# Kernel optimization log

Measured on AMD Instinct MI355X. Metric: run time of the kernel, lower is better.

The kernel has to match this reference:

```python
import jax, jax.numpy as jnp
import numpy as np

B, S, D, DK, DV = 8, 2048, 256, 128, 128

def setup_inputs() -> dict:
    key = jax.random.key(0)
    ks = jax.random.split(key, 9)
    return {
        "x_q": jax.random.normal(ks[0], (B, S, D), jnp.float32),
        "x_k": jax.random.normal(ks[1], (B, S, D), jnp.float32),
        "x_v": jax.random.normal(ks[2], (B, S, D), jnp.float32),
        "Wq": jax.random.normal(ks[3], (D, DK), jnp.float32) * (1.0 / np.sqrt(D)),
        "bq": jax.random.normal(ks[4], (DK,), jnp.float32) * 0.02,
        "Wk": jax.random.normal(ks[5], (D, DK), jnp.float32) * (1.0 / np.sqrt(D)),
        "bk": jax.random.normal(ks[6], (DK,), jnp.float32) * 0.02,
        "Wv": jax.random.normal(ks[7], (D, DV), jnp.float32) * (1.0 / np.sqrt(D)),
        "bv": jax.random.normal(ks[8], (DV,), jnp.float32) * 0.02,
    }

def reference(x_q, x_k, x_v, Wq, bq, Wk, bk, Wv, bv):
    # Dense projections: [B,S,D] @ [D,dk] + bias
    q = jnp.einsum("bsd,dk->bsk", x_q, Wq) + bq
    k = jnp.einsum("bsd,dk->bsk", x_k, Wk) + bk
    v = jnp.einsum("bsd,dv->bsv", x_v, Wv) + bv
    scale = 1.0 / np.sqrt(Wq.shape[1]).astype(np.float32)  # 1/sqrt(d_k)
    scores = jnp.einsum("bqk,bsk->bqs", q, k) * scale       # [B,S,S]
    attn = jax.nn.softmax(scores, axis=-1)
    return jnp.einsum("bqs,bsv->bqv", attn, v)               # [B,S,d_v]
```

## Files before the change

kernel.cpp:

```cpp
#include <hip/hip_runtime.h>
#include <stdint.h>

typedef float    f32x4 __attribute__((ext_vector_type(4)));
typedef _Float16 f16x8 __attribute__((ext_vector_type(8)));
typedef _Float16 f16x4 __attribute__((ext_vector_type(4)));
typedef unsigned int u32x4 __attribute__((ext_vector_type(4)));

#define SPLIT 4
#define NTILES 8

__device__ __forceinline__ f32x4 mfma16(f16x8 a, f16x8 b, f32x4 c) {
    return __builtin_amdgcn_mfma_f32_16x16x32_f16(a, b, c, 0, 0, 0);
}
__device__ __forceinline__ f32x4 mfma16k16(f16x4 a, f16x4 b, f32x4 c) {
    return __builtin_amdgcn_mfma_f32_16x16x16f16(a, b, c, 0, 0, 0);
}

__global__ __launch_bounds__(256) void prep_weights(
    const float* __restrict__ Wq, const float* __restrict__ Wk,
    const float* __restrict__ Wv, _Float16* __restrict__ wt) {
    __shared__ float Ls[64 * 65];
    const int bx = blockIdx.x;
    const int w  = bx >> 3, t = bx & 7;
    const int k0 = (t >> 1) * 64, n0 = (t & 1) * 64;
    const float* W = (w == 0) ? Wq : (w == 1) ? Wk : Wv;
    const int tid = threadIdx.x;
    #pragma unroll
    for (int i = 0; i < 16; i++) {
        int idx = i * 256 + tid;
        int r = idx >> 6, c = idx & 63;
        Ls[r * 65 + c] = W[(k0 + r) * 128 + n0 + c];
    }
    __syncthreads();
    #pragma unroll
    for (int i = 0; i < 16; i++) {
        int idx = i * 256 + tid;
        int r2 = idx >> 6, c2 = idx & 63;
        wt[w * 32768 + (n0 + r2) * 256 + k0 + c2] = (_Float16)Ls[c2 * 65 + r2];
    }
}

__global__ __launch_bounds__(256) void proj_kernel(
    const float* __restrict__ xq, const float* __restrict__ xk,
    const float* __restrict__ xv, const _Float16* __restrict__ wt,
    const float* __restrict__ bq, const float* __restrict__ bk,
    const float* __restrict__ bv,
    _Float16* __restrict__ qo, _Float16* __restrict__ ko,
    _Float16* __restrict__ vtmp)
{
    const int mode = blockIdx.y;
    const float*    X    = mode == 0 ? xq : mode == 1 ? xk : xv;
    const float*    bias = mode == 0 ? bq : mode == 1 ? bk : bv;
    const _Float16* W    = wt + mode * 32768;
    _Float16*       Y    = mode == 0 ? qo : mode == 1 ? ko : vtmp;

    const int tid  = threadIdx.x;
    const int wave = tid >> 6, lane = tid & 63;
    const int ln   = lane & 15, qd = lane >> 4;
    const int row0 = blockIdx.x * 64 + wave * 16;

    const float*    xrow = X + (size_t)(row0 + ln) * 256 + qd * 8;
    const _Float16* wb   = W + ln * 256 + qd * 8;

    f32x4 acc[8];
    #pragma unroll
    for (int i = 0; i < 8; i++) acc[i] = (f32x4){0.f, 0.f, 0.f, 0.f};

    #pragma unroll
    for (int kk = 0; kk < 8; kk++) {
        f32x4 a0 = *(const f32x4*)(xrow + kk * 32);
        f32x4 a1 = *(const f32x4*)(xrow + kk * 32 + 4);
        f16x8 af;
        af[0] = (_Float16)a0[0]; af[1] = (_Float16)a0[1];
        af[2] = (_Float16)a0[2]; af[3] = (_Float16)a0[3];
        af[4] = (_Float16)a1[0]; af[5] = (_Float16)a1[1];
        af[6] = (_Float16)a1[2]; af[7] = (_Float16)a1[3];
        #pragma unroll
        for (int nt = 0; nt < 8; nt++) {
            f16x8 bf = *(const f16x8*)(wb + nt * 4096 + kk * 32);
            acc[nt] = mfma16(af, bf, acc[nt]);
        }
    }

    const float SC = 0.08838834764831845f * 1.4426950408889634f;
    #pragma unroll
    for (int nt = 0; nt < 8; nt++) {
        int col = nt * 16 + ln;
        float bb = bias[col];
        #pragma unroll
        for (int r = 0; r < 4; r++) {
            int orow = row0 + qd * 4 + r;
            float val = acc[nt][r] + bb;
            if (mode == 0) val *= SC;
            Y[(size_t)orow * 128 + col] = (_Float16)val;
        }
    }
}

__global__ __launch_bounds__(256) void transpose_v(
    const _Float16* __restrict__ vtmp, _Float16* __restrict__ vt)
{
    __shared__ __align__(16) _Float16 Ls[64 * 72];
    const int b  = blockIdx.z;
    const int s0 = blockIdx.x * 64;
    const int d0 = blockIdx.y * 64;
    const int tid = threadIdx.x;
    #pragma unroll
    for (int i = 0; i < 2; i++) {
        int idx = i * 256 + tid;
        int r = idx >> 3, c = (idx & 7) * 8;
        *(f16x8*)&Ls[r * 72 + c] =
            *(const f16x8*)(vtmp + (size_t)(b * 2048 + s0 + r) * 128 + d0 + c);
    }
    __syncthreads();
    #pragma unroll
    for (int i = 0; i < 2; i++) {
        int idx = i * 256 + tid;
        int dr = idx >> 3, sc8 = (idx & 7) * 8;
        f16x8 o;
        #pragma unroll
        for (int j = 0; j < 8; j++) o[j] = Ls[(sc8 + j) * 72 + dr];
        *(f16x8*)(vt + (size_t)(b * 128 + d0 + dr) * 2048 + s0 + sc8) = o;
    }
}

__global__ __launch_bounds__(512, 4) void attn_kernel(
    const _Float16* __restrict__ qp, const _Float16* __restrict__ kp,
    const _Float16* __restrict__ vtp, _Float16* __restrict__ opart,
    float2* __restrict__ ml)
{
    const int bid = blockIdx.x;
    const int gx  = bid & 7;
    const int q0i = (bid >> 3) & 15;
    const int gg  = bid >> 7;
    const int g   = gg * 8 + gx;
    const int b   = g >> 2;
    const int z   = g & 3;
    const int q0  = q0i * 128;

    const int tid  = threadIdx.x;
    const int wave = tid >> 6, lane = tid & 63;
    const int ln   = lane & 15, qd = lane >> 4;

    __shared__ __align__(16) _Float16 smem[17920];
    _Float16* Ks = smem;
    _Float16* Vs = smem + 8704;

    const _Float16* qrow =
        qp + (size_t)(b * 2048 + q0 + wave * 16 + ln) * 128 + qd * 8;
    f16x8 qf[4];
    #pragma unroll
    for (int c = 0; c < 4; c++) qf[c] = *(const f16x8*)(qrow + c * 32);

    f32x4 o[8];
    #pragma unroll
    for (int i = 0; i < 8; i++) o[i] = (f32x4){0.f, 0.f, 0.f, 0.f};
    float m_run = -1e30f, l_run = 0.f;

    const _Float16* kbase = kp + (size_t)b * 2048 * 128;
    const _Float16* vbase = vtp + (size_t)b * 128 * 2048;

    for (int kt = z * NTILES; kt < z * NTILES + NTILES; kt++) {
        __syncthreads();
        const _Float16* ks = kbase + kt * 64 * 128;
        #pragma unroll
        for (int i = tid; i < 1024; i += 512) {
            int r = i >> 4, c = i & 15;
            *(u32x4*)&Ks[r * 136 + c * 8] = *(const u32x4*)(ks + r * 128 + c * 8);
        }
        const _Float16* vs = vbase + kt * 64;
        #pragma unroll
        for (int i = tid; i < 1024; i += 512) {
            int r = i >> 3, c = i & 7;
            *(u32x4*)&Vs[r * 72 + c * 8] =
                *(const u32x4*)(vs + (size_t)r * 2048 + c * 8);
        }
        __syncthreads();

        f32x4 sc[4];
        #pragma unroll
        for (int st = 0; st < 4; st++) {
            sc[st] = (f32x4){0.f, 0.f, 0.f, 0.f};
            int base = (st * 16 + ln) * 136 + qd * 8;
            #pragma unroll
            for (int c = 0; c < 4; c++) {
                f16x8 kf = *(const f16x8*)&Ks[base + c * 32];
                sc[st] = mfma16(kf, qf[c], sc[st]);
            }
        }

        float t = sc[0][0];
        #pragma unroll
        for (int st = 0; st < 4; st++)
            #pragma unroll
            for (int r = 0; r < 4; r++) t = fmaxf(t, sc[st][r]);
        t = fmaxf(t, __shfl_xor(t, 16));
        t = fmaxf(t, __shfl_xor(t, 32));
        const float mnew  = fmaxf(m_run, t);
        const float alpha = exp2f(m_run - mnew);

        f16x4 ph[4];
        float ssum = 0.f;
        #pragma unroll
        for (int st = 0; st < 4; st++) {
            #pragma unroll
            for (int r = 0; r < 4; r++) {
                float p = exp2f(sc[st][r] - mnew);
                ssum += p;
                ph[st][r] = (_Float16)p;
            }
        }
        ssum += __shfl_xor(ssum, 16);
        ssum += __shfl_xor(ssum, 32);
        l_run = l_run * alpha + ssum;
        m_run = mnew;

        #pragma unroll
        for (int dt = 0; dt < 8; dt++)
            #pragma unroll
            for (int r = 0; r < 4; r++) o[dt][r] *= alpha;

        #pragma unroll
        for (int st = 0; st < 4; st++) {
            #pragma unroll
            for (int dt = 0; dt < 8; dt++) {
                f16x4 vf = *(const f16x4*)&Vs[(dt * 16 + ln) * 72 + st * 16 + qd * 4];
                o[dt] = mfma16k16(vf, ph[st], o[dt]);
            }
        }
    }

    __syncthreads();
    _Float16* pw = smem + wave * 2176;
    #pragma unroll
    for (int dt = 0; dt < 8; dt++) {
        f16x4 h;
        #pragma unroll
        for (int r = 0; r < 4; r++) h[r] = (_Float16)o[dt][r];
        *(f16x4*)&pw[ln * 136 + dt * 16 + qd * 4] = h;
    }
    const size_t prow = (size_t)(z * 8 + b) * 2048 + q0 + wave * 16;
    __builtin_amdgcn_s_waitcnt(0);
    #pragma unroll
    for (int i = 0; i < 4; i++) {
        int row = i * 4 + qd;
        f16x8 vrow = *(const f16x8*)&pw[row * 136 + ln * 8];
        *(f16x8*)(opart + (prow + row) * 128 + ln * 8) = vrow;
    }
    if (qd == 0) {
        float2 v; v.x = m_run; v.y = l_run;
        ml[prow + ln] = v;
    }
}

__global__ __launch_bounds__(256) void merge_kernel(
    const _Float16* __restrict__ opart, const float2* __restrict__ ml,
    float* __restrict__ out)
{
    const int t = threadIdx.x;
    const int r = t >> 4, cg = t & 15;
    const size_t row = (size_t)blockIdx.x * 16 + r;

    float M = -1e30f;
    #pragma unroll
    for (int zi = 0; zi < SPLIT; zi++)
        M = fmaxf(M, ml[(size_t)zi * 16384 + row].x);
    float L = 0.f;
    float acc[8] = {0.f, 0.f, 0.f, 0.f, 0.f, 0.f, 0.f, 0.f};
    #pragma unroll
    for (int zi = 0; zi < SPLIT; zi++) {
        float2 p = ml[(size_t)zi * 16384 + row];
        float w = exp2f(p.x - M);
        L += w * p.y;
        f16x8 v = *(const f16x8*)&opart[((size_t)zi * 16384 + row) * 128 + cg * 8];
        #pragma unroll
        for (int j = 0; j < 8; j++) acc[j] += w * (float)v[j];
    }
    const float inv = 1.0f / L;
    float* op = out + row * 128 + cg * 8;
    f32x4 lo = (f32x4){acc[0] * inv, acc[1] * inv, acc[2] * inv, acc[3] * inv};
    f32x4 hi = (f32x4){acc[4] * inv, acc[5] * inv, acc[6] * inv, acc[7] * inv};
    *(f32x4*)op = lo;
    *(f32x4*)(op + 4) = hi;
}

extern "C" void kernel_launch(void* const* d_in, const int* in_sizes, int n_in,
                              void* d_out, int out_size, void* d_ws, size_t ws_size,
                              hipStream_t stream) {
    const float* xq = (const float*)d_in[0];
    const float* xk = (const float*)d_in[1];
    const float* xv = (const float*)d_in[2];
    const float* Wq = (const float*)d_in[3];
    const float* bq = (const float*)d_in[4];
    const float* Wk = (const float*)d_in[5];
    const float* bk = (const float*)d_in[6];
    const float* Wv = (const float*)d_in[7];
    const float* bv = (const float*)d_in[8];
    float* out = (float*)d_out;

    char* ws = (char*)d_ws;
    _Float16* wt    = (_Float16*)ws;
    _Float16* qo    = (_Float16*)(ws + 196608);
    _Float16* ko    = (_Float16*)(ws + 196608 + 4194304);
    _Float16* vt    = (_Float16*)(ws + 196608 + 2 * 4194304);
    float2*   ml    = (float2*)  (ws + 196608 + 3 * 4194304);
    _Float16* opart = (_Float16*)(ws + 196608 + 3 * 4194304 + 1048576);
    _Float16* vtmp  = opart;

    hipLaunchKernelGGL(prep_weights, dim3(24), dim3(256), 0, stream,
                       Wq, Wk, Wv, wt);
    hipLaunchKernelGGL(proj_kernel, dim3(256, 3), dim3(256), 0, stream,
                       xq, xk, xv, wt, bq, bk, bv, qo, ko, vtmp);
    hipLaunchKernelGGL(transpose_v, dim3(32, 2, 8), dim3(256), 0, stream,
                       vtmp, vt);
    hipLaunchKernelGGL(attn_kernel, dim3(16 * 8 * SPLIT), dim3(512), 0, stream,
                       qo, ko, vt, opart, ml);
    hipLaunchKernelGGL(merge_kernel, dim3(1024), dim3(256), 0, stream,
                       opart, ml, out);
}
```

Before: 166.9 us.

## Halve attention block size and register-prefetch next K/V tile

The attention kernel now uses 256-thread blocks covering 64 query rows, so the grid doubles to 1024 blocks. The next K and V tile is loaded from global memory into registers while the current tile is computed, hiding global load latency behind the MFMA work. The output rescale by alpha is skipped when the running max did not change anywhere in the wave. In exchange, each K/V tile is loaded from global memory by twice as many blocks, and the prefetch buffers raise register pressure.

```diff
diff --git a/kernel.cpp b/kernel.cpp
--- a/kernel.cpp
+++ b/kernel.cpp
@@ -124,19 +124,19 @@
     }
 }
 
-__global__ __launch_bounds__(512, 4) void attn_kernel(
+__global__ __launch_bounds__(256, 4) void attn_kernel(
     const _Float16* __restrict__ qp, const _Float16* __restrict__ kp,
     const _Float16* __restrict__ vtp, _Float16* __restrict__ opart,
     float2* __restrict__ ml)
 {
     const int bid = blockIdx.x;
     const int gx  = bid & 7;
-    const int q0i = (bid >> 3) & 15;
-    const int gg  = bid >> 7;
+    const int q0i = (bid >> 3) & 31;
+    const int gg  = bid >> 8;
     const int g   = gg * 8 + gx;
     const int b   = g >> 2;
     const int z   = g & 3;
-    const int q0  = q0i * 128;
+    const int q0  = q0i * 64;
 
     const int tid  = threadIdx.x;
     const int wave = tid >> 6, lane = tid & 63;
@@ -160,22 +160,38 @@
     const _Float16* kbase = kp + (size_t)b * 2048 * 128;
     const _Float16* vbase = vtp + (size_t)b * 128 * 2048;
 
-    for (int kt = z * NTILES; kt < z * NTILES + NTILES; kt++) {
+    const int kt0 = z * NTILES;
+    u32x4 kpre[4], vpre[4];
+    {
+        const _Float16* ks = kbase + (size_t)kt0 * 64 * 128;
+        const _Float16* vs = vbase + kt0 * 64;
+        #pragma unroll
+        for (int j = 0; j < 4; j++) {
+            int i = j * 256 + tid;
+            kpre[j] = *(const u32x4*)(ks + (i >> 4) * 128 + (i & 15) * 8);
+            vpre[j] = *(const u32x4*)(vs + (size_t)(i >> 3) * 2048 + (i & 7) * 8);
+        }
+    }
+
+    for (int kt = kt0; kt < kt0 + NTILES; kt++) {
         __syncthreads();
-        const _Float16* ks = kbase + kt * 64 * 128;
-        #pragma unroll
-        for (int i = tid; i < 1024; i += 512) {
-            int r = i >> 4, c = i & 15;
-            *(u32x4*)&Ks[r * 136 + c * 8] = *(const u32x4*)(ks + r * 128 + c * 8);
-        }
-        const _Float16* vs = vbase + kt * 64;
-        #pragma unroll
-        for (int i = tid; i < 1024; i += 512) {
-            int r = i >> 3, c = i & 7;
-            *(u32x4*)&Vs[r * 72 + c * 8] =
-                *(const u32x4*)(vs + (size_t)r * 2048 + c * 8);
+        #pragma unroll
+        for (int j = 0; j < 4; j++) {
+            int i = j * 256 + tid;
+            *(u32x4*)&Ks[(i >> 4) * 136 + (i & 15) * 8] = kpre[j];
+            *(u32x4*)&Vs[(i >> 3) * 72 + (i & 7) * 8]   = vpre[j];
         }
         __syncthreads();
+        if (kt + 1 < kt0 + NTILES) {
+            const _Float16* ks = kbase + (size_t)(kt + 1) * 64 * 128;
+            const _Float16* vs = vbase + (kt + 1) * 64;
+            #pragma unroll
+            for (int j = 0; j < 4; j++) {
+                int i = j * 256 + tid;
+                kpre[j] = *(const u32x4*)(ks + (i >> 4) * 128 + (i & 15) * 8);
+                vpre[j] = *(const u32x4*)(vs + (size_t)(i >> 3) * 2048 + (i & 7) * 8);
+            }
+        }
 
         f32x4 sc[4];
         #pragma unroll
@@ -215,10 +231,12 @@
         l_run = l_run * alpha + ssum;
         m_run = mnew;
 
-        #pragma unroll
-        for (int dt = 0; dt < 8; dt++)
-            #pragma unroll
-            for (int r = 0; r < 4; r++) o[dt][r] *= alpha;
+        if (__any(alpha != 1.0f)) {
+            #pragma unroll
+            for (int dt = 0; dt < 8; dt++)
+                #pragma unroll
+                for (int r = 0; r < 4; r++) o[dt][r] *= alpha;
+        }
 
         #pragma unroll
         for (int st = 0; st < 4; st++) {
@@ -313,7 +331,7 @@
                        xq, xk, xv, wt, bq, bk, bv, qo, ko, vtmp);
     hipLaunchKernelGGL(transpose_v, dim3(32, 2, 8), dim3(256), 0, stream,
                        vtmp, vt);
-    hipLaunchKernelGGL(attn_kernel, dim3(16 * 8 * SPLIT), dim3(512), 0, stream,
+    hipLaunchKernelGGL(attn_kernel, dim3(32 * 8 * SPLIT), dim3(256), 0, stream,
                        qo, ko, vt, opart, ml);
     hipLaunchKernelGGL(merge_kernel, dim3(1024), dim3(256), 0, stream,
                        opart, ml, out);
```

Measured after the change: 210.4 us. +26.1%, slower.

## Double-buffer K/V tiles via async global-to-LDS loads with XOR swizzle

Applied to the files above, without the earlier changes.

Replaces the synchronous register-staged K/V tile copies with `global_load_lds` direct-to-LDS loads into two buffers. The next tile is prefetched while the current one is computed, which also removes one barrier per iteration. LDS padding is replaced by XOR-swizzled addressing on both the store and read sides to avoid bank conflicts. Shared memory grows from about 35KB to 64KB per block, which can cut the number of resident blocks per CU and so reduce latency hiding.

```diff
diff --git a/kernel.cpp b/kernel.cpp
--- a/kernel.cpp
+++ b/kernel.cpp
@@ -14,6 +14,11 @@
 }
 __device__ __forceinline__ f32x4 mfma16k16(f16x4 a, f16x4 b, f32x4 c) {
     return __builtin_amdgcn_mfma_f32_16x16x16f16(a, b, c, 0, 0, 0);
+}
+__device__ __forceinline__ void gll16(const _Float16* g, _Float16* l) {
+    __builtin_amdgcn_global_load_lds(
+        (const __attribute__((address_space(1))) void*)g,
+        (__attribute__((address_space(3))) void*)l, 16, 0, 0);
 }
 
 __global__ __launch_bounds__(256) void prep_weights(
@@ -142,9 +147,7 @@
     const int wave = tid >> 6, lane = tid & 63;
     const int ln   = lane & 15, qd = lane >> 4;
 
-    __shared__ __align__(16) _Float16 smem[17920];
-    _Float16* Ks = smem;
-    _Float16* Vs = smem + 8704;
+    __shared__ __align__(16) _Float16 smem[32768];
 
     const _Float16* qrow =
         qp + (size_t)(b * 2048 + q0 + wave * 16 + ln) * 128 + qd * 8;
@@ -159,32 +162,41 @@
 
     const _Float16* kbase = kp + (size_t)b * 2048 * 128;
     const _Float16* vbase = vtp + (size_t)b * 128 * 2048;
-
-    for (int kt = z * NTILES; kt < z * NTILES + NTILES; kt++) {
+    const int kt0 = z * NTILES;
+
+    auto stage = [&](int kt, int buf) {
+        const _Float16* ks = kbase + (size_t)kt * 64 * 128;
+        const _Float16* vs = vbase + kt * 64;
+        _Float16* kdst0 = smem + buf * 8192;
+        _Float16* vdst0 = smem + 16384 + buf * 8192;
+        #pragma unroll
+        for (int j = 0; j < 2; j++) {
+            int p  = wave * 128 + j * 64 + lane;
+            int r  = p >> 4, cp = p & 15;
+            int cl = cp ^ (r & 15);
+            gll16(ks + r * 128 + cl * 8, kdst0 + (wave * 128 + j * 64) * 8);
+            int dv = p >> 3, cq = p & 7;
+            int c2 = cq ^ (dv & 7);
+            gll16(vs + (size_t)dv * 2048 + c2 * 8, vdst0 + (wave * 128 + j * 64) * 8);
+        }
+    };
+
+    stage(kt0, 0);
+
+    for (int it = 0; it < NTILES; it++) {
         __syncthreads();
-        const _Float16* ks = kbase + kt * 64 * 128;
-        #pragma unroll
-        for (int i = tid; i < 1024; i += 512) {
-            int r = i >> 4, c = i & 15;
-            *(u32x4*)&Ks[r * 136 + c * 8] = *(const u32x4*)(ks + r * 128 + c * 8);
-        }
-        const _Float16* vs = vbase + kt * 64;
-        #pragma unroll
-        for (int i = tid; i < 1024; i += 512) {
-            int r = i >> 3, c = i & 7;
-            *(u32x4*)&Vs[r * 72 + c * 8] =
-                *(const u32x4*)(vs + (size_t)r * 2048 + c * 8);
-        }
-        __syncthreads();
+        if (it + 1 < NTILES) stage(kt0 + it + 1, (it + 1) & 1);
+        const _Float16* kb = smem + (it & 1) * 8192;
+        const _Float16* vb = smem + 16384 + (it & 1) * 8192;
 
         f32x4 sc[4];
         #pragma unroll
         for (int st = 0; st < 4; st++) {
             sc[st] = (f32x4){0.f, 0.f, 0.f, 0.f};
-            int base = (st * 16 + ln) * 136 + qd * 8;
+            int base = (st * 16 + ln) * 128;
             #pragma unroll
             for (int c = 0; c < 4; c++) {
-                f16x8 kf = *(const f16x8*)&Ks[base + c * 32];
+                f16x8 kf = *(const f16x8*)&kb[base + ((c * 4 + qd) ^ ln) * 8];
                 sc[st] = mfma16(kf, qf[c], sc[st]);
             }
         }
@@ -224,7 +236,8 @@
         for (int st = 0; st < 4; st++) {
             #pragma unroll
             for (int dt = 0; dt < 8; dt++) {
-                f16x4 vf = *(const f16x4*)&Vs[(dt * 16 + ln) * 72 + st * 16 + qd * 4];
+                f16x4 vf = *(const f16x4*)&vb[(dt * 16 + ln) * 64 +
+                           ((st * 2 + (qd >> 1)) ^ (ln & 7)) * 8 + (qd & 1) * 4];
                 o[dt] = mfma16k16(vf, ph[st], o[dt]);
             }
         }
```

Result: no change. 164.0 us (-1.8%).
